# Optimization experiments

Hardware: AMD Instinct MI355X
Metric: run time of the kernel (lower is better)

## Reference

```python
import jax, jax.numpy as jnp
import numpy as np

# Config
V = 32000        # Y_vocab_size
EMB = 512        # decoder_embedding_size
ENC_H = 1024     # encoder_hidden_size
DEC_H = 1024     # decoder_hidden_size
ATT = 512        # attention_size
L = 2            # num_decoder_layers
B, T, S = 32, 64, 128


def setup_inputs() -> dict:
    key = jax.random.key(0)
    ks = jax.random.split(key, 20)
    s = 0.02
    emb = jax.random.normal(ks[3], (V, EMB), jnp.float32) * s
    emb = emb.at[0].set(0.0)  # padding_idx=0 row is zeros
    return {
        "y_decoder_input": jax.random.randint(ks[0], (B, T), 0, V),
        "encoder_outputs": jax.random.normal(ks[1], (B, S, ENC_H), jnp.float32),
        "decoder_init_hidden": jax.random.normal(ks[2], (L, B, DEC_H), jnp.float32),
        "encoder_mask": jnp.ones((B, S), jnp.int32),
        "emb_table": emb,
        "W_enc": jax.random.normal(ks[4], (ATT, ENC_H), jnp.float32) * s,
        "W_dec": jax.random.normal(ks[5], (ATT, DEC_H), jnp.float32) * s,
        "v_w": jax.random.normal(ks[6], (ATT,), jnp.float32) * s,
        "W_ih0": jax.random.normal(ks[7], (DEC_H, EMB + ENC_H), jnp.float32) * s,
        "W_hh0": jax.random.normal(ks[8], (DEC_H, DEC_H), jnp.float32) * s,
        "b_ih0": jax.random.normal(ks[9], (DEC_H,), jnp.float32) * s,
        "b_hh0": jax.random.normal(ks[10], (DEC_H,), jnp.float32) * s,
        "W_ih1": jax.random.normal(ks[11], (DEC_H, DEC_H), jnp.float32) * s,
        "W_hh1": jax.random.normal(ks[12], (DEC_H, DEC_H), jnp.float32) * s,
        "b_ih1": jax.random.normal(ks[13], (DEC_H,), jnp.float32) * s,
        "b_hh1": jax.random.normal(ks[14], (DEC_H,), jnp.float32) * s,
        "fc_w": jax.random.normal(ks[15], (V - 1, DEC_H), jnp.float32) * s,
        "fc_b": jnp.zeros((V - 1,), jnp.float32),
    }


def reference(y_decoder_input, encoder_outputs, decoder_init_hidden, encoder_mask,
              emb_table, W_enc, W_dec, v_w,
              W_ih0, W_hh0, b_ih0, b_hh0, W_ih1, W_hh1, b_ih1, b_hh1,
              fc_w, fc_b):
    embedded = emb_table[y_decoder_input]                       # [B,T,EMB]
    enc_proj = jnp.einsum('bse,ae->bsa', encoder_outputs, W_enc)  # hoisted (same math each step)
    pad_mask = (encoder_mask == 0)                              # [B,S]

    def step(hidden, emb_t):
        prev = hidden[-1]                                       # [B,DEC_H] top layer
        dec_p = prev @ W_dec.T                                  # [B,ATT]
        scores = jnp.tanh(enc_proj + dec_p[:, None, :]) @ v_w   # [B,S]
        scores = jnp.where(pad_mask, jnp.float32(-1e9), scores)
        attn = jax.nn.softmax(scores, axis=-1)                  # [B,S]
        context = jnp.einsum('bs,bse->be', attn, encoder_outputs)  # [B,ENC_H]
        x = jnp.concatenate([emb_t, context], axis=1)           # [B,EMB+ENC_H]
        h0 = jnp.tanh(x @ W_ih0.T + b_ih0 + hidden[0] @ W_hh0.T + b_hh0)
        h1 = jnp.tanh(h0 @ W_ih1.T + b_ih1 + hidden[1] @ W_hh1.T + b_hh1)
        out = h1 @ fc_w.T + fc_b                                # [B,V-1]
        return jnp.stack([h0, h1]), (out, attn)

    _, (outs, attns) = jax.lax.scan(step, decoder_init_hidden,
                                    jnp.swapaxes(embedded, 0, 1))  # scan over T
    outputs = jnp.swapaxes(outs, 0, 1)                          # [B,T,V-1]
    attn_weights = jnp.swapaxes(attns, 0, 1)                    # [B,T,S]
    return outputs, attn_weights
```

## Files before the change

### kernel.cpp

```cpp
#include <hip/hip_runtime.h>

typedef unsigned short u16;
typedef unsigned int u32;
typedef __attribute__((ext_vector_type(8))) short bf16x8;
typedef __attribute__((ext_vector_type(4))) float f32x4;

#define MFMA_BF16(a,b,c) __builtin_amdgcn_mfma_f32_16x16x32_bf16((a),(b),(c),0,0,0)

__device__ __forceinline__ u16 f2bf(float f) {
  union { float f; u32 u; } v; v.f = f;
  u32 r = v.u + 0x7FFFu + ((v.u >> 16) & 1u);
  return (u16)(r >> 16);
}
__device__ __forceinline__ float bf2f(u16 h) {
  union { u32 u; float f; } v; v.u = ((u32)h) << 16; return v.f;
}
__device__ __forceinline__ float tanh_fast(float x) {
  float e = __expf(2.0f * x);
  return 1.0f - 2.0f / (e + 1.0f);
}
__device__ __forceinline__ float exp2_fast(float x) {
  float r; asm("v_exp_f32 %0, %1" : "=v"(r) : "v"(x)); return r;
}
__device__ __forceinline__ float rcp_fast(float x) {
  float r; asm("v_rcp_f32 %0, %1" : "=v"(r) : "v"(x)); return r;
}

__device__ __forceinline__ void issue_lcoh(bf16x8& v, const u16* p) {
  asm volatile("global_load_dwordx4 %0, %1, off sc0 sc1" : "=v"(v) : "v"(p));
}
__device__ __forceinline__ void issue_lcoh_f4(f32x4& v, const float* p) {
  asm volatile("global_load_dwordx4 %0, %1, off sc0 sc1" : "=v"(v) : "v"(p));
}
__device__ __forceinline__ void issue_lcoh_u32(u32& v, const u32* p) {
  asm volatile("global_load_dword %0, %1, off sc0 sc1" : "=v"(v) : "v"(p));
}
__device__ __forceinline__ void vm_wait0() {
  asm volatile("s_waitcnt vmcnt(0)" ::: "memory");
  __builtin_amdgcn_sched_barrier(0);
}
__device__ __forceinline__ void scoh_f32(float* p, float v) {
  asm volatile("global_store_dword %0, %1, off sc0 sc1" :: "v"(p), "v"(v) : "memory");
}
__device__ __forceinline__ void scoh_u32(u32* p, u32 v) {
  asm volatile("global_store_dword %0, %1, off sc0 sc1" :: "v"(p), "v"(v) : "memory");
}
__device__ __forceinline__ void scoh_u16(u16* p, u16 v) {
  u32 w = v;
  asm volatile("global_store_short %0, %1, off sc0 sc1" :: "v"(p), "v"(w) : "memory");
}
__device__ __forceinline__ u32 poll_load(const u32* p) {
  u32 v;
  asm volatile("global_load_dword %0, %1, off sc0 sc1\n\ts_waitcnt vmcnt(0)"
               : "=v"(v) : "v"(p) : "memory");
  return v;
}

__device__ __forceinline__ void poll_flags(const u32* base, int P, u32 target) {
  if ((threadIdx.x >> 6) == 0) {
    const int lane = threadIdx.x & 63;
    if (P == 128) {
      const u32* s0 = base + (size_t)lane * 32;
      const u32* s1 = base + (size_t)(lane + 64) * 32;
      for (;;) {
        u32 v0, v1;
        asm volatile("global_load_dword %0, %2, off sc0 sc1\n\t"
                     "global_load_dword %1, %3, off sc0 sc1\n\t"
                     "s_waitcnt vmcnt(0)"
                     : "=v"(v0), "=v"(v1) : "v"(s0), "v"(s1) : "memory");
        if (__all((v0 >= target) && (v1 >= target))) break;
        __builtin_amdgcn_s_sleep(2);
      }
    } else {
      const u32* s0 = base + (size_t)(lane & (P - 1)) * 32;
      for (;;) {
        u32 v0 = poll_load(s0);
        if (__all(v0 >= target)) break;
        __builtin_amdgcn_s_sleep(2);
      }
    }
  }
  __syncthreads();
  __builtin_amdgcn_sched_barrier(0);
}
__device__ __forceinline__ void post_flag(u32* slot, u32 val) {
  asm volatile("s_waitcnt vmcnt(0)" ::: "memory");
  __syncthreads();
  if (threadIdx.x == 0) scoh_u32(slot, val);
}

__global__ void prep_kernel(
    const float* __restrict__ fcw, const float* __restrict__ enc,
    const float* __restrict__ wenc, const float* __restrict__ wdec,
    const float* __restrict__ wih0, const float* __restrict__ whh0,
    const float* __restrict__ wih1, const float* __restrict__ whh1,
    const float* __restrict__ bih0, const float* __restrict__ bhh0,
    const float* __restrict__ bih1, const float* __restrict__ bhh1,
    const float* __restrict__ emb, const int* __restrict__ yin,
    const float* __restrict__ dih,
    u16* __restrict__ fcwb, u16* __restrict__ encb, u16* __restrict__ wencb,
    u16* __restrict__ wdecb, u16* __restrict__ w0eh, u16* __restrict__ w0ctx,
    u16* __restrict__ w1cat, u16* __restrict__ embbt,
    float* __restrict__ bias0, float* __restrict__ bias1,
    u16* __restrict__ h0buf0, u16* __restrict__ h1buf0)
{
  const float SCL = 2.8853900817779268f;
  const long long total = 43845632LL;
  for (long long i = (long long)blockIdx.x * 256 + threadIdx.x; i < total;
       i += (long long)gridDim.x * 256) {
    if (i < 32768000LL) {
      int r = (int)(i >> 10), c = (int)(i & 1023);
      fcwb[i] = (r < 31999) ? f2bf(fcw[(long long)r * 1024 + c]) : (u16)0;
    } else if (i < 36962304LL) {
      long long j = i - 32768000LL; encb[j] = f2bf(enc[j]);
    } else if (i < 37486592LL) {
      long long j = i - 36962304LL; wencb[j] = f2bf(wenc[j] * SCL);
    } else if (i < 38010880LL) {
      long long j = i - 37486592LL; wdecb[j] = f2bf(wdec[j] * SCL);
    } else if (i < 39583744LL) {
      long long j = i - 38010880LL;
      int r = (int)(j / 1536), c = (int)(j % 1536);
      float v = (c < 512) ? wih0[(long long)r * 1536 + c]
                          : whh0[(long long)r * 1024 + (c - 512)];
      w0eh[j] = f2bf(v);
    } else if (i < 40632320LL) {
      long long j = i - 39583744LL;
      int r = (int)(j >> 10), e = (int)(j & 1023);
      w0ctx[j] = f2bf(wih0[(long long)r * 1536 + 512 + e]);
    } else if (i < 42729472LL) {
      long long j = i - 40632320LL;
      int r = (int)(j >> 11), c = (int)(j & 2047);
      w1cat[j] = f2bf(c < 1024 ? wih1[(r << 10) + c] : whh1[(r << 10) + (c - 1024)]);
    } else if (i < 43778048LL) {
      long long j = i - 42729472LL;
      int bt = (int)(j >> 9), c = (int)(j & 511);
      int y = yin[bt];
      embbt[j] = f2bf(emb[(long long)y * 512 + c]);
    } else if (i < 43779072LL) {
      int j = (int)(i - 43778048LL); bias0[j] = bih0[j] + bhh0[j];
    } else if (i < 43780096LL) {
      int j = (int)(i - 43779072LL); bias1[j] = bih1[j] + bhh1[j];
    } else if (i < 43812864LL) {
      int j = (int)(i - 43780096LL); h0buf0[j] = f2bf(dih[j]);
    } else {
      int j = (int)(i - 43812864LL); h1buf0[j] = f2bf(dih[32768 + j]);
    }
  }
}

template <int OUT16>
__global__ __launch_bounds__(256) void gemm128(
    const u16* __restrict__ A, const u16* __restrict__ Bm,
    const float* __restrict__ bias, void* __restrict__ Cv,
    int K, int ldc, int Nvalid, int ntN)
{
  __shared__ u16 As[128 * 32];
  __shared__ u16 Bs[128 * 32];
  const int tid = threadIdx.x;
  const int bid = blockIdx.x;
  const int tM = bid / ntN, tN = bid - tM * ntN;
  const int m0 = tM * 128, n0 = tN * 128;
  const int lane = tid & 63, wid = tid >> 6;
  const int wm = wid >> 1, wn = wid & 1;
  const int srow = tid >> 1, scol = (tid & 1) * 16;

  const u16* gA = A + (size_t)(m0 + srow) * K + scol;
  const u16* gB = Bm + (size_t)(n0 + srow) * K + scol;
  u16* sA = &As[srow * 32 + scol];
  u16* sB = &Bs[srow * 32 + scol];

  f32x4 acc[4][4];
#pragma unroll
  for (int i = 0; i < 4; ++i)
#pragma unroll
    for (int j = 0; j < 4; ++j) acc[i][j] = (f32x4){0, 0, 0, 0};

  const int aoff = (wm * 64 + (lane & 15)) * 32 + ((lane >> 4) << 3);
  const int boff = (wn * 64 + (lane & 15)) * 32 + ((lane >> 4) << 3);

  for (int k0 = 0; k0 < K; k0 += 32) {
    bf16x8 va0 = *(const bf16x8*)(gA + k0);
    bf16x8 va1 = *(const bf16x8*)(gA + k0 + 8);
    bf16x8 vb0 = *(const bf16x8*)(gB + k0);
    bf16x8 vb1 = *(const bf16x8*)(gB + k0 + 8);
    __syncthreads();
    *((bf16x8*)sA) = va0;  *((bf16x8*)(sA + 8)) = va1;
    *((bf16x8*)sB) = vb0;  *((bf16x8*)(sB + 8)) = vb1;
    __syncthreads();
    bf16x8 af[4], bfj[4];
#pragma unroll
    for (int i = 0; i < 4; ++i) af[i] = *(const bf16x8*)&As[aoff + i * 512];
#pragma unroll
    for (int j = 0; j < 4; ++j) bfj[j] = *(const bf16x8*)&Bs[boff + j * 512];
#pragma unroll
    for (int i = 0; i < 4; ++i)
#pragma unroll
      for (int j = 0; j < 4; ++j)
        acc[i][j] = MFMA_BF16(af[i], bfj[j], acc[i][j]);
  }

#pragma unroll
  for (int i = 0; i < 4; ++i) {
#pragma unroll
    for (int j = 0; j < 4; ++j) {
      int row = m0 + wm * 64 + i * 16 + ((lane >> 4) << 2);
      int cc = n0 + wn * 64 + j * 16 + (lane & 15);
      if (cc < Nvalid) {
        float bs = bias ? bias[cc] : 0.f;
#pragma unroll
        for (int jj = 0; jj < 4; ++jj) {
          if (OUT16)
            ((u16*)Cv)[(size_t)(row + jj) * ldc + cc] = f2bf(acc[i][j][jj] + bs);
          else
            ((float*)Cv)[(size_t)(row + jj) * ldc + cc] = acc[i][j][jj] + bs;
        }
      }
    }
  }
}

__global__ __launch_bounds__(512, 1) void decoder_persistent(
    const u16* __restrict__ wdecb, const u16* __restrict__ w0eh,
    const u16* __restrict__ w1cat, const u16* __restrict__ encprojb,
    const u16* __restrict__ encW0T, const u16* __restrict__ embbt,
    const float* __restrict__ bias0, const float* __restrict__ bias1,
    const float* __restrict__ vw, const int* __restrict__ msk,
    u16* __restrict__ partials, float* __restrict__ attbuf,
    u16* __restrict__ h0buf, u16* __restrict__ h1buf,
    u16* __restrict__ h1all, float* __restrict__ outattn, u32* flags)
{
  extern __shared__ char smem[];
  const int tid = threadIdx.x;
  const int bid = blockIdx.x;
  const int lane = tid & 63, wid = tid >> 6;
  const f32x4 zero4 = {0, 0, 0, 0};

  if (bid < 64) {
    const int hh = bid, n0 = hh * 16;
    u16* w1L = (u16*)smem;
    u16* wdL = (u16*)(smem + 65536);
    u16* h1newL = (u16*)(smem + 98304);
    float* scr = (float*)(smem + 100352);
    float* b1L = (float*)(smem + 116736);
    {
      for (int c = tid; c < 4096; c += 512)
        *(bf16x8*)&w1L[c * 8] = *(const bf16x8*)&w1cat[(size_t)n0 * 2048 + c * 8];
      bf16x8 r0 = *(const bf16x8*)&wdecb[(size_t)tid * 1024 + n0];
      bf16x8 r1 = *(const bf16x8*)&wdecb[(size_t)tid * 1024 + n0 + 8];
      bf16x8 z = {0, 0, 0, 0, 0, 0, 0, 0};
      *(bf16x8*)&wdL[tid * 32] = r0;
      *(bf16x8*)&wdL[tid * 32 + 8] = r1;
      *(bf16x8*)&wdL[tid * 32 + 16] = z;
      *(bf16x8*)&wdL[tid * 32 + 24] = z;
      h1newL[tid] = 0; h1newL[512 + tid] = 0;
      if (tid < 16) b1L[tid] = bias1[n0 + tid];
    }
    __syncthreads();
    {
      int b = tid >> 4, n = tid & 15;
      h1newL[b * 32 + n] = h1buf[(size_t)b * 1024 + n0 + n];
    }
    __syncthreads();

    for (int t = -1; t < 64; ++t) {
      if (t >= 0) {
        poll_flags(flags, 64, (u32)(t + 1));
        const u16* hp = h1buf + (size_t)(t & 1) * 32768;
        f32x4 acc[2] = {zero4, zero4};
        {
          bf16x8 av[8];
#pragma unroll
          for (int mt = 0; mt < 2; ++mt)
#pragma unroll
            for (int i = 0; i < 4; ++i) {
              int b = mt * 16 + (lane & 15);
              int k = (wid * 4 + i) * 32 + ((lane >> 4) << 3);
              issue_lcoh(av[mt * 4 + i], hp + (size_t)b * 1024 + k);
            }
          vm_wait0();
#pragma unroll
          for (int mt = 0; mt < 2; ++mt)
#pragma unroll
            for (int i = 0; i < 4; ++i) {
              int n = lane & 15;
              int k = (wid * 4 + i) * 32 + ((lane >> 4) << 3);
              acc[mt] = MFMA_BF16(av[mt * 4 + i],
                                  *(const bf16x8*)&w1L[n * 2048 + 1024 + k], acc[mt]);
            }
        }
        poll_flags(flags + 96 * 32, 128, (u32)(t + 1));
        const u16* hn = h0buf + (size_t)((t + 1) & 1) * 32768;
        {
          bf16x8 av[8];
#pragma unroll
          for (int mt = 0; mt < 2; ++mt)
#pragma unroll
            for (int i = 0; i < 4; ++i) {
              int b = mt * 16 + (lane & 15);
              int k = (wid * 4 + i) * 32 + ((lane >> 4) << 3);
              issue_lcoh(av[mt * 4 + i], hn + (size_t)b * 1024 + k);
            }
          vm_wait0();
#pragma unroll
          for (int mt = 0; mt < 2; ++mt)
#pragma unroll
            for (int i = 0; i < 4; ++i) {
              int n = lane & 15;
              int k = (wid * 4 + i) * 32 + ((lane >> 4) << 3);
              acc[mt] = MFMA_BF16(av[mt * 4 + i],
                                  *(const bf16x8*)&w1L[n * 2048 + k], acc[mt]);
            }
        }
        *(f32x4*)&scr[((wid * 2 + 0) * 64 + lane) * 4] = acc[0];
        *(f32x4*)&scr[((wid * 2 + 1) * 64 + lane) * 4] = acc[1];
        __syncthreads();
        {
          int b = tid >> 4, n = tid & 15;
          int lanep = ((b & 15) >> 2) * 16 + n, r = b & 3, mt = b >> 4;
          float s = b1L[n];
#pragma unroll
          for (int w = 0; w < 8; ++w) s += scr[((w * 2 + mt) * 64 + lanep) * 4 + r];
          u16 v = f2bf(tanh_fast(s));
          h1newL[b * 32 + n] = v;
          scoh_u16(h1buf + (size_t)((t + 1) & 1) * 32768 + (size_t)b * 1024 + n0 + n, v);
          h1all[(size_t)(b * 64 + t) * 1024 + n0 + n] = v;
        }
        __syncthreads();
      }
      {
#pragma unroll
        for (int mt = 0; mt < 2; ++mt) {
          bf16x8 a = *(const bf16x8*)&h1newL[(mt * 16 + (lane & 15)) * 32 + ((lane >> 4) << 3)];
#pragma unroll
          for (int i = 0; i < 4; ++i) {
            int nt = wid * 4 + i;
            bf16x8 bb = *(const bf16x8*)&wdL[(nt * 16 + (lane & 15)) * 32 + ((lane >> 4) << 3)];
            f32x4 c = MFMA_BF16(a, bb, zero4);
            int a0 = nt * 16 + (lane & 15);
#pragma unroll
            for (int j = 0; j < 4; ++j) {
              int b = mt * 16 + ((lane >> 4) << 2) + j;
              scoh_u16(partials + ((size_t)b * 64 + hh) * 512 + a0, f2bf(c[j]));
            }
          }
        }
      }
      post_flag(flags + (size_t)hh * 32, (u32)(t + 2));
    }
  } else if (bid < 96) {
    const int b = bid - 64;
    u16* epL = (u16*)smem;
    float* vwL = (float*)(smem + 133120);
    float* decp2 = (float*)(smem + 135168);
    float* decpL = (float*)(smem + 139264);
    float* eL = (float*)(smem + 141312);
    float* mkL = (float*)(smem + 141824);
    float* sumL = (float*)(smem + 142336);
    {
      for (int c = tid; c < 8192; c += 512)
        *(bf16x8*)&epL[(c >> 6) * 520 + (c & 63) * 8] =
            *(const bf16x8*)&encprojb[((size_t)b * 128 + (c >> 6)) * 512 + (c & 63) * 8];
      vwL[tid] = vw[tid];
      if (tid < 128) mkL[tid] = (float)msk[b * 128 + tid];
    }
    __syncthreads();
    for (int t = 0; t < 64; ++t) {
      poll_flags(flags, 64, (u32)(t + 1));
      {
        const int a2 = tid & 255, ph = tid >> 8;
        const u32* pb = (const u32*)partials + (size_t)b * 16384 + (size_t)ph * 32 * 256 + a2;
        float acc0 = 0.f, acc1 = 0.f;
        u32 wv[16];
#pragma unroll
        for (int g = 0; g < 2; ++g) {
#pragma unroll
          for (int i = 0; i < 16; ++i)
            issue_lcoh_u32(wv[i], pb + (size_t)(g * 16 + i) * 256);
          vm_wait0();
#pragma unroll
          for (int i = 0; i < 16; ++i) {
            acc0 += bf2f((u16)(wv[i] & 0xffffu));
            acc1 += bf2f((u16)(wv[i] >> 16));
          }
        }
        decp2[ph * 512 + a2 * 2] = acc0;
        decp2[ph * 512 + a2 * 2 + 1] = acc1;
      }
      __syncthreads();
      decpL[tid] = decp2[tid] + decp2[512 + tid];
      __syncthreads();
      {
        const int s = tid >> 2, q = tid & 3;
        const u16* ep = &epL[s * 520 + q * 128];
        const float* dp = &decpL[q * 128];
        const float* vv = &vwL[q * 128];
        float a0 = 0.f, a1 = 0.f;
#pragma unroll
        for (int ii = 0; ii < 16; ++ii) {
          int i = (ii + q * 4) & 15;
          bf16x8 ev = *(const bf16x8*)(ep + i * 8);
#pragma unroll
          for (int e = 0; e < 8; e += 2) {
            float x0 = bf2f((u16)ev[e]) + dp[i * 8 + e];
            float x1 = bf2f((u16)ev[e + 1]) + dp[i * 8 + e + 1];
            a0 = fmaf(vv[i * 8 + e],     1.f - 2.f * rcp_fast(exp2_fast(x0) + 1.f), a0);
            a1 = fmaf(vv[i * 8 + e + 1], 1.f - 2.f * rcp_fast(exp2_fast(x1) + 1.f), a1);
          }
        }
        float acc = a0 + a1;
        acc += __shfl_xor(acc, 1);
        acc += __shfl_xor(acc, 2);
        float e = 0.f;
        if (q == 0) { e = (mkL[s] != 0.f) ? __expf(acc) : 0.f; eL[s] = e; }
        float ee = e;
#pragma unroll
        for (int off = 1; off < 64; off <<= 1) ee += __shfl_xor(ee, off);
        if (lane == 0) sumL[wid] = ee;
      }
      __syncthreads();
      {
        float tot = sumL[0] + sumL[1] + sumL[2] + sumL[3] +
                    sumL[4] + sumL[5] + sumL[6] + sumL[7];
        if (tid < 128) {
          float att = (tot > 0.f) ? eL[tid] * rcp_fast(tot) : 0.0078125f;
          outattn[(size_t)(b * 64 + t) * 128 + tid] = att;
          scoh_f32(attbuf + b * 128 + tid, att);
        }
      }
      post_flag(flags + (size_t)bid * 32, (u32)(t + 1));
    }
  } else {
    const int h = bid - 96, j0 = h * 8;
    u16* w0L = (u16*)smem;
    u16* e0L = (u16*)(smem + 49152);
    float* attL = (float*)(smem + 118912);
    float* scrH = (float*)(smem + 135296);
    float* attP = (float*)(smem + 151680);
    float* b0L = (float*)(smem + 152704);
    {
      for (int c = tid; c < 1536; c += 512) {
        int j = c / 192, off = (c % 192) * 8;
        *(bf16x8*)&w0L[j * 1536 + off] = *(const bf16x8*)&w0eh[(size_t)(j0 + j) * 1536 + off];
      }
      for (int c = tid; c < 4096; c += 512) {
        int j = c >> 9, rem = c & 511, bb = rem >> 4, so = (rem & 15) * 8;
        *(bf16x8*)&e0L[j * 4360 + bb * 136 + so] =
            *(const bf16x8*)&encW0T[(size_t)(j0 + j) * 4096 + bb * 128 + so];
      }
      if (tid < 8) b0L[tid] = bias0[j0 + tid];
    }
    __syncthreads();
    for (int t = 0; t < 64; ++t) {
      poll_flags(flags + 96 * 32, 128, (u32)t);
      f32x4 acc[2] = {zero4, zero4};
      {
        bf16x8 ave[4], avh[8];
#pragma unroll
        for (int mt = 0; mt < 2; ++mt)
#pragma unroll
          for (int i = 0; i < 2; ++i) {
            int b = mt * 16 + (lane & 15);
            int k = (wid * 2 + i) * 32 + ((lane >> 4) << 3);
            ave[mt * 2 + i] = *(const bf16x8*)&embbt[((size_t)b * 64 + t) * 512 + k];
          }
        const u16* hp = h0buf + (size_t)(t & 1) * 32768;
#pragma unroll
        for (int mt = 0; mt < 2; ++mt)
#pragma unroll
          for (int i = 0; i < 4; ++i) {
            int b = mt * 16 + (lane & 15);
            int k = (wid * 4 + i) * 32 + ((lane >> 4) << 3);
            issue_lcoh(avh[mt * 4 + i], hp + (size_t)b * 1024 + k);
          }
        vm_wait0();
#pragma unroll
        for (int mt = 0; mt < 2; ++mt) {
#pragma unroll
          for (int i = 0; i < 2; ++i) {
            int n = lane & 15;
            int k = (wid * 2 + i) * 32 + ((lane >> 4) << 3);
            acc[mt] = MFMA_BF16(ave[mt * 2 + i], *(const bf16x8*)&w0L[n * 1536 + k], acc[mt]);
          }
#pragma unroll
          for (int i = 0; i < 4; ++i) {
            int n = lane & 15;
            int k = (wid * 4 + i) * 32 + ((lane >> 4) << 3);
            acc[mt] = MFMA_BF16(avh[mt * 4 + i],
                                *(const bf16x8*)&w0L[n * 1536 + 512 + k], acc[mt]);
          }
        }
        *(f32x4*)&scrH[((wid * 2 + 0) * 64 + lane) * 4] = acc[0];
        *(f32x4*)&scrH[((wid * 2 + 1) * 64 + lane) * 4] = acc[1];
      }
      poll_flags(flags + 64 * 32, 32, (u32)(t + 1));
      {
        f32x4 v0, v1;
        issue_lcoh_f4(v0, attbuf + tid * 8);
        issue_lcoh_f4(v1, attbuf + tid * 8 + 4);
        vm_wait0();
        *(f32x4*)&attL[tid * 8] = v0;
        *(f32x4*)&attL[tid * 8 + 4] = v1;
      }
      __syncthreads();
      {
        int b = tid >> 4, j = (tid >> 1) & 7, h2 = tid & 1;
        const u16* ep = &e0L[j * 4360 + b * 136 + h2 * 64];
        const float* ar = &attL[b * 128 + h2 * 64];
        float a2 = 0.f;
#pragma unroll
        for (int c8 = 0; c8 < 8; ++c8) {
          bf16x8 ev = *(const bf16x8*)(ep + c8 * 8);
#pragma unroll
          for (int e = 0; e < 8; ++e) a2 = fmaf(ar[c8 * 8 + e], bf2f((u16)ev[e]), a2);
        }
        a2 += __shfl_xor(a2, 1);
        if (h2 == 0) attP[b * 8 + j] = a2;
      }
      __syncthreads();
      if (tid < 256) {
        int b = tid >> 3, j = tid & 7;
        int lanep = ((b & 15) >> 2) * 16 + j, r = b & 3, mt = b >> 4;
        float s = attP[b * 8 + j] + b0L[j];
#pragma unroll
        for (int w = 0; w < 8; ++w) s += scrH[((w * 2 + mt) * 64 + lanep) * 4 + r];
        u16 v = f2bf(tanh_fast(s));
        scoh_u16(h0buf + (size_t)((t + 1) & 1) * 32768 + (size_t)b * 1024 + j0 + j, v);
      }
      post_flag(flags + (size_t)bid * 32, (u32)(t + 1));
    }
  }
}

extern "C" void kernel_launch(void* const* d_in, const int* in_sizes, int n_in,
                              void* d_out, int out_size, void* d_ws, size_t ws_size,
                              hipStream_t stream)
{
  const int*   yin  = (const int*)d_in[0];
  const float* enc  = (const float*)d_in[1];
  const float* dih  = (const float*)d_in[2];
  const int*   msk  = (const int*)d_in[3];
  const float* emb  = (const float*)d_in[4];
  const float* wenc = (const float*)d_in[5];
  const float* wdec = (const float*)d_in[6];
  const float* vw   = (const float*)d_in[7];
  const float* wih0 = (const float*)d_in[8];
  const float* whh0 = (const float*)d_in[9];
  const float* bih0 = (const float*)d_in[10];
  const float* bhh0 = (const float*)d_in[11];
  const float* wih1 = (const float*)d_in[12];
  const float* whh1 = (const float*)d_in[13];
  const float* bih1 = (const float*)d_in[14];
  const float* bhh1 = (const float*)d_in[15];
  const float* fcw  = (const float*)d_in[16];
  const float* fcb  = (const float*)d_in[17];

  char* ws = (char*)d_ws;
  size_t off = 0;
  auto alloc = [&](size_t bytes) {
    char* p = ws + off; off += (bytes + 255) & ~(size_t)255; return p;
  };
  u16*   fcwb     = (u16*)alloc(32768000ULL * 2);
  u16*   encb     = (u16*)alloc(4194304ULL * 2);
  u16*   wencb    = (u16*)alloc(524288ULL * 2);
  u16*   wdecb    = (u16*)alloc(524288ULL * 2);
  u16*   w0eh     = (u16*)alloc(1572864ULL * 2);
  u16*   w0ctx    = (u16*)alloc(1048576ULL * 2);
  u16*   w1cat    = (u16*)alloc(2097152ULL * 2);
  u16*   embbt    = (u16*)alloc(1048576ULL * 2);
  u16*   encprojb = (u16*)alloc(2097152ULL * 2);
  u16*   encW0T   = (u16*)alloc(4194304ULL * 2);
  u16*   partials = (u16*)alloc(1048576ULL * 2);
  float* attbuf   = (float*)alloc(4096ULL * 4);
  u16*   h0buf    = (u16*)alloc(65536ULL * 2);
  u16*   h1buf    = (u16*)alloc(65536ULL * 2);
  u16*   h1all    = (u16*)alloc(2097152ULL * 2);
  float* bias0    = (float*)alloc(1024ULL * 4);
  float* bias1    = (float*)alloc(1024ULL * 4);
  u32*   flags    = (u32*)alloc(32768ULL);
  if (off > ws_size) return;

  float* outlog  = (float*)d_out;
  float* outattn = outlog + 65533952ULL;

  (void)hipMemsetAsync(flags, 0, 32768, stream);

  prep_kernel<<<2048, 256, 0, stream>>>(
      fcw, enc, wenc, wdec, wih0, whh0, wih1, whh1,
      bih0, bhh0, bih1, bhh1, emb, yin, dih,
      fcwb, encb, wencb, wdecb, w0eh, w0ctx, w1cat, embbt, bias0, bias1,
      h0buf, h1buf);

  gemm128<1><<<32 * 4, 256, 0, stream>>>(encb, wencb, nullptr, encprojb,
                                         1024, 512, 512, 4);
  gemm128<1><<<8 * 32, 256, 0, stream>>>(w0ctx, encb, nullptr, encW0T,
                                         1024, 4096, 4096, 32);

  (void)hipFuncSetAttribute((const void*)decoder_persistent,
                            hipFuncAttributeMaxDynamicSharedMemorySize, 153600);
  decoder_persistent<<<224, 512, 153600, stream>>>(
      wdecb, w0eh, w1cat, encprojb, encW0T, embbt, bias0, bias1,
      vw, msk, partials, attbuf, h0buf, h1buf, h1all, outattn, flags);

  gemm128<0><<<16 * 250, 256, 0, stream>>>(h1all, fcwb, fcb, outlog,
                                           1024, 31999, 31999, 250);
}
```

Measured before the change: 1.770 ms.

## Repartition persistent decoder into fewer, wider block roles with vectorized coherent stores

Measured after the change: 1.933 ms. 1.09x slower.

```diff
diff --git a/kernel.cpp b/kernel.cpp
--- a/kernel.cpp
+++ b/kernel.cpp
@@ -4,6 +4,7 @@
 typedef unsigned int u32;
 typedef __attribute__((ext_vector_type(8))) short bf16x8;
 typedef __attribute__((ext_vector_type(4))) float f32x4;
+typedef __attribute__((ext_vector_type(2))) unsigned int u32x2;
 
 #define MFMA_BF16(a,b,c) __builtin_amdgcn_mfma_f32_16x16x32_bf16((a),(b),(c),0,0,0)
 
@@ -29,25 +30,19 @@
 __device__ __forceinline__ void issue_lcoh(bf16x8& v, const u16* p) {
   asm volatile("global_load_dwordx4 %0, %1, off sc0 sc1" : "=v"(v) : "v"(p));
 }
-__device__ __forceinline__ void issue_lcoh_f4(f32x4& v, const float* p) {
-  asm volatile("global_load_dwordx4 %0, %1, off sc0 sc1" : "=v"(v) : "v"(p));
-}
-__device__ __forceinline__ void issue_lcoh_u32(u32& v, const u32* p) {
-  asm volatile("global_load_dword %0, %1, off sc0 sc1" : "=v"(v) : "v"(p));
-}
 __device__ __forceinline__ void vm_wait0() {
   asm volatile("s_waitcnt vmcnt(0)" ::: "memory");
   __builtin_amdgcn_sched_barrier(0);
 }
-__device__ __forceinline__ void scoh_f32(float* p, float v) {
-  asm volatile("global_store_dword %0, %1, off sc0 sc1" :: "v"(p), "v"(v) : "memory");
-}
 __device__ __forceinline__ void scoh_u32(u32* p, u32 v) {
   asm volatile("global_store_dword %0, %1, off sc0 sc1" :: "v"(p), "v"(v) : "memory");
 }
-__device__ __forceinline__ void scoh_u16(u16* p, u16 v) {
-  u32 w = v;
-  asm volatile("global_store_short %0, %1, off sc0 sc1" :: "v"(p), "v"(w) : "memory");
+__device__ __forceinline__ void scoh_dx2(u16* p, u32 lo, u32 hi) {
+  u32x2 v; v.x = lo; v.y = hi;
+  asm volatile("global_store_dwordx2 %0, %1, off sc0 sc1" :: "v"(p), "v"(v) : "memory");
+}
+__device__ __forceinline__ void scoh_dx4(u16* p, bf16x8 v) {
+  asm volatile("global_store_dwordx4 %0, %1, off sc0 sc1" :: "v"(p), "v"(v) : "memory");
 }
 __device__ __forceinline__ u32 poll_load(const u32* p) {
   u32 v;
@@ -57,27 +52,14 @@
 }
 
 __device__ __forceinline__ void poll_flags(const u32* base, int P, u32 target) {
+  if (target == 0u) return;
   if ((threadIdx.x >> 6) == 0) {
     const int lane = threadIdx.x & 63;
-    if (P == 128) {
-      const u32* s0 = base + (size_t)lane * 32;
-      const u32* s1 = base + (size_t)(lane + 64) * 32;
-      for (;;) {
-        u32 v0, v1;
-        asm volatile("global_load_dword %0, %2, off sc0 sc1\n\t"
-                     "global_load_dword %1, %3, off sc0 sc1\n\t"
-                     "s_waitcnt vmcnt(0)"
-                     : "=v"(v0), "=v"(v1) : "v"(s0), "v"(s1) : "memory");
-        if (__all((v0 >= target) && (v1 >= target))) break;
-        __builtin_amdgcn_s_sleep(2);
-      }
-    } else {
-      const u32* s0 = base + (size_t)(lane & (P - 1)) * 32;
-      for (;;) {
-        u32 v0 = poll_load(s0);
-        if (__all(v0 >= target)) break;
-        __builtin_amdgcn_s_sleep(2);
-      }
+    const u32* s0 = base + (size_t)(lane & (P - 1)) * 32;
+    for (;;) {
+      u32 v0 = poll_load(s0);
+      if (__all(v0 >= target)) break;
+      __builtin_amdgcn_s_sleep(1);
     }
   }
   __syncthreads();
@@ -225,7 +207,7 @@
     const u16* __restrict__ encW0T, const u16* __restrict__ embbt,
     const float* __restrict__ bias0, const float* __restrict__ bias1,
     const float* __restrict__ vw, const int* __restrict__ msk,
-    u16* __restrict__ partials, float* __restrict__ attbuf,
+    u16* __restrict__ partials, u16* __restrict__ attbufB,
     u16* __restrict__ h0buf, u16* __restrict__ h1buf,
     u16* __restrict__ h1all, float* __restrict__ outattn, u32* flags)
 {
@@ -233,129 +215,122 @@
   const int tid = threadIdx.x;
   const int bid = blockIdx.x;
   const int lane = tid & 63, wid = tid >> 6;
+  const int l15 = lane & 15, l16 = (lane >> 4) << 3;
   const f32x4 zero4 = {0, 0, 0, 0};
-
-  if (bid < 64) {
-    const int hh = bid, n0 = hh * 16;
+  u32* h1flags = flags;
+  u32* scflags = flags + 32 * 32;
+  u32* h0flags = flags + 64 * 32;
+
+  if (bid < 32) {
+    const int n0 = bid * 32;
     u16* w1L = (u16*)smem;
-    u16* wdL = (u16*)(smem + 65536);
-    u16* h1newL = (u16*)(smem + 98304);
-    float* scr = (float*)(smem + 100352);
-    float* b1L = (float*)(smem + 116736);
+    float* scr = (float*)(smem + 131584);
+    u16* h1newL = (u16*)(smem + 147968);
+    float* b1L = (float*)(smem + 150016);
     {
-      for (int c = tid; c < 4096; c += 512)
-        *(bf16x8*)&w1L[c * 8] = *(const bf16x8*)&w1cat[(size_t)n0 * 2048 + c * 8];
-      bf16x8 r0 = *(const bf16x8*)&wdecb[(size_t)tid * 1024 + n0];
-      bf16x8 r1 = *(const bf16x8*)&wdecb[(size_t)tid * 1024 + n0 + 8];
-      bf16x8 z = {0, 0, 0, 0, 0, 0, 0, 0};
-      *(bf16x8*)&wdL[tid * 32] = r0;
-      *(bf16x8*)&wdL[tid * 32 + 8] = r1;
-      *(bf16x8*)&wdL[tid * 32 + 16] = z;
-      *(bf16x8*)&wdL[tid * 32 + 24] = z;
-      h1newL[tid] = 0; h1newL[512 + tid] = 0;
-      if (tid < 16) b1L[tid] = bias1[n0 + tid];
+      for (int c = tid; c < 8192; c += 512) {
+        int r = c >> 8, seg = (c & 255) * 8;
+        *(bf16x8*)&w1L[r * 2056 + seg] =
+            *(const bf16x8*)&w1cat[(size_t)(n0 + r) * 2048 + seg];
+      }
+      if (tid < 32) b1L[tid] = bias1[n0 + tid];
+      for (int c = tid; c < 1024; c += 512) {
+        int b = c >> 5, n = c & 31;
+        h1newL[c] = h1buf[(size_t)b * 1024 + n0 + n];
+      }
     }
     __syncthreads();
-    {
-      int b = tid >> 4, n = tid & 15;
-      h1newL[b * 32 + n] = h1buf[(size_t)b * 1024 + n0 + n];
-    }
-    __syncthreads();
+    const int bt = wid >> 2, kq = wid & 3;
+    const int ab = bt * 16 + l15;
 
     for (int t = -1; t < 64; ++t) {
       if (t >= 0) {
-        poll_flags(flags, 64, (u32)(t + 1));
+        poll_flags(h1flags, 32, (u32)(t + 1));
         const u16* hp = h1buf + (size_t)(t & 1) * 32768;
-        f32x4 acc[2] = {zero4, zero4};
+        f32x4 acc0 = zero4, acc1 = zero4;
         {
           bf16x8 av[8];
 #pragma unroll
-          for (int mt = 0; mt < 2; ++mt)
-#pragma unroll
-            for (int i = 0; i < 4; ++i) {
-              int b = mt * 16 + (lane & 15);
-              int k = (wid * 4 + i) * 32 + ((lane >> 4) << 3);
-              issue_lcoh(av[mt * 4 + i], hp + (size_t)b * 1024 + k);
-            }
+          for (int ks = 0; ks < 8; ++ks)
+            issue_lcoh(av[ks], hp + (size_t)ab * 1024 + kq * 256 + ks * 32 + l16);
           vm_wait0();
 #pragma unroll
-          for (int mt = 0; mt < 2; ++mt)
-#pragma unroll
-            for (int i = 0; i < 4; ++i) {
-              int n = lane & 15;
-              int k = (wid * 4 + i) * 32 + ((lane >> 4) << 3);
-              acc[mt] = MFMA_BF16(av[mt * 4 + i],
-                                  *(const bf16x8*)&w1L[n * 2048 + 1024 + k], acc[mt]);
-            }
-        }
-        poll_flags(flags + 96 * 32, 128, (u32)(t + 1));
+          for (int ks = 0; ks < 8; ++ks) {
+            int kx = 1024 + kq * 256 + ks * 32 + l16;
+            acc0 = MFMA_BF16(av[ks], *(const bf16x8*)&w1L[l15 * 2056 + kx], acc0);
+            acc1 = MFMA_BF16(av[ks], *(const bf16x8*)&w1L[(16 + l15) * 2056 + kx], acc1);
+          }
+        }
+        poll_flags(h0flags, 64, (u32)(t + 1));
         const u16* hn = h0buf + (size_t)((t + 1) & 1) * 32768;
         {
           bf16x8 av[8];
 #pragma unroll
-          for (int mt = 0; mt < 2; ++mt)
-#pragma unroll
-            for (int i = 0; i < 4; ++i) {
-              int b = mt * 16 + (lane & 15);
-              int k = (wid * 4 + i) * 32 + ((lane >> 4) << 3);
-              issue_lcoh(av[mt * 4 + i], hn + (size_t)b * 1024 + k);
-            }
+          for (int ks = 0; ks < 8; ++ks)
+            issue_lcoh(av[ks], hn + (size_t)ab * 1024 + kq * 256 + ks * 32 + l16);
           vm_wait0();
 #pragma unroll
-          for (int mt = 0; mt < 2; ++mt)
-#pragma unroll
-            for (int i = 0; i < 4; ++i) {
-              int n = lane & 15;
-              int k = (wid * 4 + i) * 32 + ((lane >> 4) << 3);
-              acc[mt] = MFMA_BF16(av[mt * 4 + i],
-                                  *(const bf16x8*)&w1L[n * 2048 + k], acc[mt]);
-            }
-        }
-        *(f32x4*)&scr[((wid * 2 + 0) * 64 + lane) * 4] = acc[0];
-        *(f32x4*)&scr[((wid * 2 + 1) * 64 + lane) * 4] = acc[1];
+          for (int ks = 0; ks < 8; ++ks) {
+            int kx = kq * 256 + ks * 32 + l16;
+            acc0 = MFMA_BF16(av[ks], *(const bf16x8*)&w1L[l15 * 2056 + kx], acc0);
+            acc1 = MFMA_BF16(av[ks], *(const bf16x8*)&w1L[(16 + l15) * 2056 + kx], acc1);
+          }
+        }
+        *(f32x4*)&scr[((wid * 2 + 0) * 64 + lane) * 4] = acc0;
+        *(f32x4*)&scr[((wid * 2 + 1) * 64 + lane) * 4] = acc1;
         __syncthreads();
         {
-          int b = tid >> 4, n = tid & 15;
-          int lanep = ((b & 15) >> 2) * 16 + n, r = b & 3, mt = b >> 4;
-          float s = b1L[n];
-#pragma unroll
-          for (int w = 0; w < 8; ++w) s += scr[((w * 2 + mt) * 64 + lanep) * 4 + r];
-          u16 v = f2bf(tanh_fast(s));
-          h1newL[b * 32 + n] = v;
-          scoh_u16(h1buf + (size_t)((t + 1) & 1) * 32768 + (size_t)b * 1024 + n0 + n, v);
-          h1all[(size_t)(b * 64 + t) * 1024 + n0 + n] = v;
+          int b = tid >> 4, n16 = tid & 15;
+          int lanep = (((b & 15) >> 2) << 4) | n16;
+          int r = b & 3, btc = b >> 4;
+#pragma unroll
+          for (int nt = 0; nt < 2; ++nt) {
+            int n = nt * 16 + n16;
+            float s = b1L[n];
+#pragma unroll
+            for (int q = 0; q < 4; ++q)
+              s += scr[(((btc * 4 + q) * 2 + nt) * 64 + lanep) * 4 + r];
+            h1newL[b * 32 + n] = f2bf(tanh_fast(s));
+          }
         }
         __syncthreads();
-      }
-      {
-#pragma unroll
-        for (int mt = 0; mt < 2; ++mt) {
-          bf16x8 a = *(const bf16x8*)&h1newL[(mt * 16 + (lane & 15)) * 32 + ((lane >> 4) << 3)];
+        if (tid < 128) {
+          int b = tid >> 2, q = tid & 3;
+          bf16x8 v8 = *(const bf16x8*)&h1newL[b * 32 + q * 8];
+          scoh_dx4(h1buf + (size_t)((t + 1) & 1) * 32768 + (size_t)b * 1024 + n0 + q * 8, v8);
+          *(bf16x8*)(h1all + ((size_t)b * 64 + t) * 1024 + n0 + q * 8) = v8;
+        }
+      }
+      {
+#pragma unroll
+        for (int bt2 = 0; bt2 < 2; ++bt2) {
+          bf16x8 hb = *(const bf16x8*)&h1newL[(bt2 * 16 + l15) * 32 + l16];
 #pragma unroll
           for (int i = 0; i < 4; ++i) {
-            int nt = wid * 4 + i;
-            bf16x8 bb = *(const bf16x8*)&wdL[(nt * 16 + (lane & 15)) * 32 + ((lane >> 4) << 3)];
-            f32x4 c = MFMA_BF16(a, bb, zero4);
-            int a0 = nt * 16 + (lane & 15);
-#pragma unroll
-            for (int j = 0; j < 4; ++j) {
-              int b = mt * 16 + ((lane >> 4) << 2) + j;
-              scoh_u16(partials + ((size_t)b * 64 + hh) * 512 + a0, f2bf(c[j]));
-            }
+            int at = wid * 4 + i;
+            bf16x8 wa = *(const bf16x8*)&wdecb[(size_t)(at * 16 + l15) * 1024 + n0 + l16];
+            f32x4 c = MFMA_BF16(wa, hb, zero4);
+            int a0 = at * 16 + ((lane >> 4) << 2);
+            int bb = bt2 * 16 + l15;
+            u32 lo = (u32)f2bf(c[0]) | ((u32)f2bf(c[1]) << 16);
+            u32 hi = (u32)f2bf(c[2]) | ((u32)f2bf(c[3]) << 16);
+            scoh_dx2(partials + ((size_t)bb * 32 + bid) * 512 + a0, lo, hi);
           }
         }
       }
-      post_flag(flags + (size_t)hh * 32, (u32)(t + 2));
-    }
-  } else if (bid < 96) {
-    const int b = bid - 64;
+      post_flag(h1flags + (size_t)bid * 32, (u32)(t + 2));
+    }
+  } else if (bid < 64) {
+    const int b = bid - 32;
     u16* epL = (u16*)smem;
     float* vwL = (float*)(smem + 133120);
-    float* decp2 = (float*)(smem + 135168);
-    float* decpL = (float*)(smem + 139264);
-    float* eL = (float*)(smem + 141312);
-    float* mkL = (float*)(smem + 141824);
-    float* sumL = (float*)(smem + 142336);
+    float* red = (float*)(smem + 135168);
+    float* decpL = (float*)(smem + 151552);
+    float* attF = (float*)(smem + 153600);
+    u16* attB = (u16*)(smem + 154112);
+    float* eL = (float*)(smem + 154368);
+    float* mkL = (float*)(smem + 154880);
+    float* sumL = (float*)(smem + 155392);
     {
       for (int c = tid; c < 8192; c += 512)
         *(bf16x8*)&epL[(c >> 6) * 520 + (c & 63) * 8] =
@@ -365,29 +340,31 @@
     }
     __syncthreads();
     for (int t = 0; t < 64; ++t) {
-      poll_flags(flags, 64, (u32)(t + 1));
-      {
-        const int a2 = tid & 255, ph = tid >> 8;
-        const u32* pb = (const u32*)partials + (size_t)b * 16384 + (size_t)ph * 32 * 256 + a2;
-        float acc0 = 0.f, acc1 = 0.f;
-        u32 wv[16];
-#pragma unroll
-        for (int g = 0; g < 2; ++g) {
-#pragma unroll
-          for (int i = 0; i < 16; ++i)
-            issue_lcoh_u32(wv[i], pb + (size_t)(g * 16 + i) * 256);
-          vm_wait0();
-#pragma unroll
-          for (int i = 0; i < 16; ++i) {
-            acc0 += bf2f((u16)(wv[i] & 0xffffu));
-            acc1 += bf2f((u16)(wv[i] >> 16));
-          }
-        }
-        decp2[ph * 512 + a2 * 2] = acc0;
-        decp2[ph * 512 + a2 * 2 + 1] = acc1;
+      poll_flags(h1flags, 32, (u32)(t + 1));
+      {
+        const int a8 = tid & 63, hg = tid >> 6;
+        const int a = a8 * 8;
+        bf16x8 w[4];
+#pragma unroll
+        for (int i = 0; i < 4; ++i)
+          issue_lcoh(w[i], partials + ((size_t)b * 32 + hg * 4 + i) * 512 + a);
+        vm_wait0();
+        float s[8];
+#pragma unroll
+        for (int e = 0; e < 8; ++e) {
+          s[e] = bf2f((u16)w[0][e]) + bf2f((u16)w[1][e]) +
+                 bf2f((u16)w[2][e]) + bf2f((u16)w[3][e]);
+        }
+#pragma unroll
+        for (int e = 0; e < 8; ++e) red[hg * 512 + a + e] = s[e];
       }
       __syncthreads();
-      decpL[tid] = decp2[tid] + decp2[512 + tid];
+      {
+        float s = 0.f;
+#pragma unroll
+        for (int hg = 0; hg < 8; ++hg) s += red[hg * 512 + tid];
+        decpL[tid] = s;
+      }
       __syncthreads();
       {
         const int s = tid >> 2, q = tid & 3;
@@ -423,110 +400,90 @@
                     sumL[4] + sumL[5] + sumL[6] + sumL[7];
         if (tid < 128) {
           float att = (tot > 0.f) ? eL[tid] * rcp_fast(tot) : 0.0078125f;
-          outattn[(size_t)(b * 64 + t) * 128 + tid] = att;
-          scoh_f32(attbuf + b * 128 + tid, att);
-        }
-      }
-      post_flag(flags + (size_t)bid * 32, (u32)(t + 1));
+          attF[tid] = att;
+          attB[tid] = f2bf(att);
+        }
+      }
+      __syncthreads();
+      if (tid < 32)
+        *(f32x4*)(outattn + ((size_t)b * 64 + t) * 128 + tid * 4) = *(const f32x4*)&attF[tid * 4];
+      if (tid < 16)
+        scoh_dx4(attbufB + (size_t)b * 128 + tid * 8, *(const bf16x8*)&attB[tid * 8]);
+      post_flag(scflags + (size_t)b * 32, (u32)(t + 1));
     }
   } else {
-    const int h = bid - 96, j0 = h * 8;
-    u16* w0L = (u16*)smem;
-    u16* e0L = (u16*)(smem + 49152);
-    float* attL = (float*)(smem + 118912);
-    float* scrH = (float*)(smem + 135296);
-    float* attP = (float*)(smem + 151680);
-    float* b0L = (float*)(smem + 152704);
+    const int h = bid - 64, j0 = h * 16;
+    u16* e0L = (u16*)smem;
+    float* attL = (float*)(smem + 131328);
+    float* scrH = (float*)(smem + 147712);
+    u16* h0newL = (u16*)(smem + 155904);
+    float* b0L = (float*)(smem + 156928);
     {
-      for (int c = tid; c < 1536; c += 512) {
-        int j = c / 192, off = (c % 192) * 8;
-        *(bf16x8*)&w0L[j * 1536 + off] = *(const bf16x8*)&w0eh[(size_t)(j0 + j) * 1536 + off];
-      }
-      for (int c = tid; c < 4096; c += 512) {
-        int j = c >> 9, rem = c & 511, bb = rem >> 4, so = (rem & 15) * 8;
-        *(bf16x8*)&e0L[j * 4360 + bb * 136 + so] =
-            *(const bf16x8*)&encW0T[(size_t)(j0 + j) * 4096 + bb * 128 + so];
-      }
-      if (tid < 8) b0L[tid] = bias0[j0 + tid];
+      for (int c = tid; c < 8192; c += 512) {
+        int j = c >> 9, off = (c & 511) * 8;
+        *(bf16x8*)&e0L[j * 4104 + off] =
+            *(const bf16x8*)&encW0T[(size_t)(j0 + j) * 4096 + off];
+      }
+      if (tid < 16) b0L[tid] = bias0[j0 + tid];
     }
     __syncthreads();
+    const int bt = wid >> 2, kq = wid & 3;
+    const int ab = bt * 16 + l15;
+
     for (int t = 0; t < 64; ++t) {
-      poll_flags(flags + 96 * 32, 128, (u32)t);
-      f32x4 acc[2] = {zero4, zero4};
-      {
-        bf16x8 ave[4], avh[8];
-#pragma unroll
-        for (int mt = 0; mt < 2; ++mt)
-#pragma unroll
-          for (int i = 0; i < 2; ++i) {
-            int b = mt * 16 + (lane & 15);
-            int k = (wid * 2 + i) * 32 + ((lane >> 4) << 3);
-            ave[mt * 2 + i] = *(const bf16x8*)&embbt[((size_t)b * 64 + t) * 512 + k];
-          }
+      poll_flags(h0flags, 64, (u32)t);
+      {
+        bf16x8 xa[12], wb[12];
         const u16* hp = h0buf + (size_t)(t & 1) * 32768;
 #pragma unroll
-        for (int mt = 0; mt < 2; ++mt)
-#pragma unroll
-          for (int i = 0; i < 4; ++i) {
-            int b = mt * 16 + (lane & 15);
-            int k = (wid * 4 + i) * 32 + ((lane >> 4) << 3);
-            issue_lcoh(avh[mt * 4 + i], hp + (size_t)b * 1024 + k);
-          }
+        for (int ks = 0; ks < 12; ++ks) {
+          int kk = kq * 384 + ks * 32;
+          if (kk < 512)
+            xa[ks] = *(const bf16x8*)&embbt[((size_t)ab * 64 + t) * 512 + kk + l16];
+          else
+            issue_lcoh(xa[ks], hp + (size_t)ab * 1024 + (kk - 512) + l16);
+          wb[ks] = *(const bf16x8*)&w0eh[(size_t)(j0 + l15) * 1536 + kk + l16];
+        }
         vm_wait0();
-#pragma unroll
-        for (int mt = 0; mt < 2; ++mt) {
-#pragma unroll
-          for (int i = 0; i < 2; ++i) {
-            int n = lane & 15;
-            int k = (wid * 2 + i) * 32 + ((lane >> 4) << 3);
-            acc[mt] = MFMA_BF16(ave[mt * 2 + i], *(const bf16x8*)&w0L[n * 1536 + k], acc[mt]);
-          }
-#pragma unroll
-          for (int i = 0; i < 4; ++i) {
-            int n = lane & 15;
-            int k = (wid * 4 + i) * 32 + ((lane >> 4) << 3);
-            acc[mt] = MFMA_BF16(avh[mt * 4 + i],
-                                *(const bf16x8*)&w0L[n * 1536 + 512 + k], acc[mt]);
-          }
-        }
-        *(f32x4*)&scrH[((wid * 2 + 0) * 64 + lane) * 4] = acc[0];
-        *(f32x4*)&scrH[((wid * 2 + 1) * 64 + lane) * 4] = acc[1];
-      }
-      poll_flags(flags + 64 * 32, 32, (u32)(t + 1));
-      {
-        f32x4 v0, v1;
-        issue_lcoh_f4(v0, attbuf + tid * 8);
-        issue_lcoh_f4(v1, attbuf + tid * 8 + 4);
+        f32x4 acc = zero4;
+#pragma unroll
+        for (int ks = 0; ks < 12; ++ks) acc = MFMA_BF16(xa[ks], wb[ks], acc);
+        *(f32x4*)&scrH[(wid * 64 + lane) * 4] = acc;
+      }
+      poll_flags(scflags, 32, (u32)(t + 1));
+      {
+        bf16x8 v;
+        issue_lcoh(v, attbufB + tid * 8);
         vm_wait0();
-        *(f32x4*)&attL[tid * 8] = v0;
-        *(f32x4*)&attL[tid * 8 + 4] = v1;
+#pragma unroll
+        for (int e = 0; e < 8; ++e) attL[tid * 8 + e] = bf2f((u16)v[e]);
       }
       __syncthreads();
       {
-        int b = tid >> 4, j = (tid >> 1) & 7, h2 = tid & 1;
-        const u16* ep = &e0L[j * 4360 + b * 136 + h2 * 64];
-        const float* ar = &attL[b * 128 + h2 * 64];
-        float a2 = 0.f;
-#pragma unroll
-        for (int c8 = 0; c8 < 8; ++c8) {
-          bf16x8 ev = *(const bf16x8*)(ep + c8 * 8);
-#pragma unroll
-          for (int e = 0; e < 8; ++e) a2 = fmaf(ar[c8 * 8 + e], bf2f((u16)ev[e]), a2);
-        }
-        a2 += __shfl_xor(a2, 1);
-        if (h2 == 0) attP[b * 8 + j] = a2;
+        int b = tid >> 4, j = tid & 15;
+        const float* ar = &attL[b * 128];
+        float adot = 0.f;
+#pragma unroll
+        for (int c8 = 0; c8 < 16; ++c8) {
+          bf16x8 ev = *(const bf16x8*)&e0L[j * 4104 + b * 128 + c8 * 8];
+#pragma unroll
+          for (int e = 0; e < 8; ++e) adot = fmaf(ar[c8 * 8 + e], bf2f((u16)ev[e]), adot);
+        }
+        int lanep = (((b & 15) >> 2) << 4) | j;
+        int r = b & 3, btc = b >> 4;
+        float s = adot + b0L[j];
+#pragma unroll
+        for (int q = 0; q < 4; ++q)
+          s += scrH[((btc * 4 + q) * 64 + lanep) * 4 + r];
+        h0newL[b * 16 + j] = f2bf(tanh_fast(s));
       }
       __syncthreads();
-      if (tid < 256) {
-        int b = tid >> 3, j = tid & 7;
-        int lanep = ((b & 15) >> 2) * 16 + j, r = b & 3, mt = b >> 4;
-        float s = attP[b * 8 + j] + b0L[j];
-#pragma unroll
-        for (int w = 0; w < 8; ++w) s += scrH[((w * 2 + mt) * 64 + lanep) * 4 + r];
-        u16 v = f2bf(tanh_fast(s));
-        scoh_u16(h0buf + (size_t)((t + 1) & 1) * 32768 + (size_t)b * 1024 + j0 + j, v);
-      }
-      post_flag(flags + (size_t)bid * 32, (u32)(t + 1));
+      if (tid < 64) {
+        int b = tid >> 1, half = tid & 1;
+        scoh_dx4(h0buf + (size_t)((t + 1) & 1) * 32768 + (size_t)b * 1024 + j0 + half * 8,
+                 *(const bf16x8*)&h0newL[b * 16 + half * 8]);
+      }
+      post_flag(h0flags + (size_t)h * 32, (u32)(t + 1));
     }
   }
 }
@@ -569,20 +526,20 @@
   u16*   embbt    = (u16*)alloc(1048576ULL * 2);
   u16*   encprojb = (u16*)alloc(2097152ULL * 2);
   u16*   encW0T   = (u16*)alloc(4194304ULL * 2);
-  u16*   partials = (u16*)alloc(1048576ULL * 2);
-  float* attbuf   = (float*)alloc(4096ULL * 4);
+  u16*   partials = (u16*)alloc(524288ULL * 2);
+  u16*   attbufB  = (u16*)alloc(4096ULL * 2);
   u16*   h0buf    = (u16*)alloc(65536ULL * 2);
   u16*   h1buf    = (u16*)alloc(65536ULL * 2);
   u16*   h1all    = (u16*)alloc(2097152ULL * 2);
   float* bias0    = (float*)alloc(1024ULL * 4);
   float* bias1    = (float*)alloc(1024ULL * 4);
-  u32*   flags    = (u32*)alloc(32768ULL);
+  u32*   flags    = (u32*)alloc(16384ULL);
   if (off > ws_size) return;
 
   float* outlog  = (float*)d_out;
   float* outattn = outlog + 65533952ULL;
 
-  (void)hipMemsetAsync(flags, 0, 32768, stream);
+  (void)hipMemsetAsync(flags, 0, 16384, stream);
 
   prep_kernel<<<2048, 256, 0, stream>>>(
       fcw, enc, wenc, wdec, wih0, whh0, wih1, whh1,
@@ -596,10 +553,10 @@
                                          1024, 4096, 4096, 32);
 
   (void)hipFuncSetAttribute((const void*)decoder_persistent,
-                            hipFuncAttributeMaxDynamicSharedMemorySize, 153600);
-  decoder_persistent<<<224, 512, 153600, stream>>>(
+                            hipFuncAttributeMaxDynamicSharedMemorySize, 157184);
+  decoder_persistent<<<128, 512, 157184, stream>>>(
       wdecb, w0eh, w1cat, encprojb, encW0T, embbt, bias0, bias1,
-      vw, msk, partials, attbuf, h0buf, h1buf, h1all, outattn, flags);
+      vw, msk, partials, attbufB, h0buf, h1buf, h1all, outattn, flags);
 
   gemm128<0><<<16 * 250, 256, 0, stream>>>(h1all, fcwb, fcb, outlog,
                                            1024, 31999, 31999, 250);
```
